# Performance work log

Measured on AMD Instinct MI355X. Metric: run time of the kernel, lower is better.

Reference implementation:

```python
import jax, jax.numpy as jnp
import numpy as np

N, E, H, XD, ED, YD, L = 10000, 640000, 128, 8, 8, 112, 4
EPS_MSG = 1e-7   # GENConv message eps
EPS_SM = 1e-16   # pyg softmax denom eps
EPS_LN = 1e-5    # layernorm eps


def node_ln(x, g, b):
    # torch.nn.LayerNorm over last dim
    m = x.mean(axis=-1, keepdims=True)
    v = x.var(axis=-1, keepdims=True)
    return (x - m) * jax.lax.rsqrt(v + EPS_LN) * g + b


def graph_ln(x, g, b):
    # pyg LayerNorm mode='graph' (no batch): global mean/std over all nodes+channels
    xc = x - x.mean()
    std = jnp.sqrt((xc * xc).mean())
    return xc / (std + EPS_LN) * g + b


def setup_inputs() -> dict:
    key = jax.random.key(0)
    ks = jax.random.split(key, 10)
    rn = lambda k, s, sc: jax.random.normal(k, s, jnp.float32) * sc
    return {
        "x": jax.random.normal(ks[0], (N, XD), jnp.float32),
        "edge_index": jax.random.randint(ks[1], (2, E), 0, N),
        "edge_attr": jax.random.normal(ks[2], (E, ED), jnp.float32),
        "Wn": rn(ks[3], (XD, H), 0.3), "bn": jnp.zeros((H,), jnp.float32),
        "We": rn(ks[4], (ED, H), 0.3), "be": jnp.zeros((H,), jnp.float32),
        "t": jnp.ones((L,), jnp.float32),
        "W1": rn(ks[5], (L, H, 2 * H), 0.08), "b1": jnp.zeros((L, 2 * H), jnp.float32),
        "g1": jnp.ones((L, 2 * H), jnp.float32), "bt1": jnp.zeros((L, 2 * H), jnp.float32),
        "W2": rn(ks[6], (L, 2 * H, H), 0.08), "b2": jnp.zeros((L, H), jnp.float32),
        "lng": jnp.ones((L, H), jnp.float32), "lnb": jnp.zeros((L, H), jnp.float32),
        "Wout": rn(ks[7], (H, YD), 0.08), "bout": jnp.zeros((YD,), jnp.float32),
    }


def reference(x, edge_index, edge_attr, Wn, bn, We, be, t, W1, b1, g1, bt1,
              W2, b2, lng, lnb, Wout, bout):
    src, dst = edge_index[0], edge_index[1]
    h = x @ Wn + bn                       # [N,H] node encoder
    ea = edge_attr @ We + be              # [E,H] edge encoder

    def gen_conv(h, i):
        msg = jax.nn.relu(h[src] + ea) + EPS_MSG          # [E,H]
        logit = msg * t[i]
        mx = jax.ops.segment_max(logit, dst, num_segments=N)
        ex = jnp.exp(logit - mx[dst])
        den = jax.ops.segment_sum(ex, dst, num_segments=N)
        alpha = ex / (den[dst] + EPS_SM)
        agg = jax.ops.segment_sum(alpha * msg, dst, num_segments=N) + h  # root add
        z = jax.nn.relu(graph_ln(agg @ W1[i] + b1[i], g1[i], bt1[i]))
        return z @ W2[i] + b2[i]

    h = gen_conv(h, 0)                    # first layer: conv only
    for i in range(1, L):                 # res+ blocks (dropout off: eval)
        r = jax.nn.relu(node_ln(h, lng[i], lnb[i]))
        h = h + gen_conv(r, i)
    h = jax.nn.relu(node_ln(h, lng[0], lnb[0]))  # layers[0].act(layers[0].norm(x))
    return h @ Wout + bout
```

## Files before the change

kernel.cpp:

```cpp
#include <hip/hip_runtime.h>
#include <math.h>

#define NN 10000
#define NE 640000
#define H 128
#define H2 256
#define XD 8
#define ED 8
#define YD 112
#define NL 4
#define EPS_MSG 1e-7f
#define EPS_SM 1e-16f
#define EPS_LN 1e-5f
#define TN 16
#define NB1 (NN / TN)

__global__ void hist_k(const int* __restrict__ dst, int* __restrict__ counts) {
    int e = blockIdx.x * 256 + threadIdx.x;
    if (e < NE) atomicAdd(&counts[dst[e]], 1);
}

__global__ void scan_k(const int* __restrict__ counts, int* __restrict__ rowptr) {
    __shared__ int part[1024];
    int tid = threadIdx.x;
    const int CH = (NN + 1023) / 1024;
    int base = tid * CH;
    int s = 0;
    for (int j = 0; j < CH; j++) { int i = base + j; if (i < NN) s += counts[i]; }
    part[tid] = s; __syncthreads();
    for (int off = 1; off < 1024; off <<= 1) {
        int v = (tid >= off) ? part[tid - off] : 0;
        __syncthreads();
        part[tid] += v;
        __syncthreads();
    }
    int run = part[tid] - s;
    for (int j = 0; j < CH; j++) {
        int i = base + j;
        if (i < NN) { rowptr[i] = run; run += counts[i]; }
    }
    if (tid == 1023) rowptr[NN] = run;
}

__global__ void scatter_k(const int* __restrict__ src, const int* __restrict__ dst,
                          const float* __restrict__ eattr, const int* __restrict__ rowptr,
                          int* __restrict__ fill, int* __restrict__ srcs,
                          _Float16* __restrict__ eacsr) {
    int e = blockIdx.x * 256 + threadIdx.x;
    if (e >= NE) return;
    int d = dst[e];
    int pos = rowptr[d] + atomicAdd(&fill[d], 1);
    srcs[pos] = src[e];
    const float4* ein = (const float4*)eattr;
    float4 a = ein[(size_t)e * 2];
    float4 b = ein[(size_t)e * 2 + 1];
    float4 pack;
    _Float16* pp = (_Float16*)&pack;
    pp[0] = (_Float16)a.x; pp[1] = (_Float16)a.y; pp[2] = (_Float16)a.z; pp[3] = (_Float16)a.w;
    pp[4] = (_Float16)b.x; pp[5] = (_Float16)b.y; pp[6] = (_Float16)b.z; pp[7] = (_Float16)b.w;
    ((float4*)eacsr)[pos] = pack;
}

__global__ void node_enc_k(const float* __restrict__ x, const float* __restrict__ Wn,
                           const float* __restrict__ bn, float* __restrict__ h) {
    int n = blockIdx.x, c = threadIdx.x;
    __shared__ float xl[XD];
    if (c < XD) xl[c] = x[n * XD + c];
    __syncthreads();
    float acc = bn[c];
#pragma unroll
    for (int k = 0; k < XD; k++) acc = fmaf(xl[k], Wn[k * H + c], acc);
    h[(size_t)n * H + c] = acc;
}

__global__ void __launch_bounds__(128) edge_agg_k(
    const float* __restrict__ rin, const int* __restrict__ rowptr,
    const int* __restrict__ srcs, const _Float16* __restrict__ eacsr,
    const float* __restrict__ We, const float* __restrict__ be,
    const float* __restrict__ tptr, int layer, float* __restrict__ agg) {
    int n = blockIdx.x, c = threadIdx.x;
    float wc[ED];
#pragma unroll
    for (int k = 0; k < ED; k++) wc[k] = We[k * H + c];
    float bec = be[c];
    float ts2 = tptr[layer] * 1.44269504088896f;
    int beg = rowptr[n], end = rowptr[n + 1];
    float rv = rin[(size_t)n * H + c];
    float den = 0.f, num = 0.f;
#pragma unroll 4
    for (int j = beg; j < end; ++j) {
        int sn = srcs[j];
        float4 raw = *(const float4*)(eacsr + (size_t)j * ED);
        const _Float16* ep = (const _Float16*)&raw;
        float hv = rin[(size_t)sn * H + c];
        float p = bec;
        p = fmaf((float)ep[0], wc[0], p); p = fmaf((float)ep[1], wc[1], p);
        p = fmaf((float)ep[2], wc[2], p); p = fmaf((float)ep[3], wc[3], p);
        p = fmaf((float)ep[4], wc[4], p); p = fmaf((float)ep[5], wc[5], p);
        p = fmaf((float)ep[6], wc[6], p); p = fmaf((float)ep[7], wc[7], p);
        float msg = fmaxf(hv + p, 0.f) + EPS_MSG;
        float pe = __builtin_amdgcn_exp2f(msg * ts2);
        den += pe;
        num = fmaf(pe, msg, num);
    }
    agg[(size_t)n * H + c] = num / (den + EPS_SM) + rv;
}

__global__ void __launch_bounds__(256) mm1_k(const float* __restrict__ agg,
    const float* __restrict__ W1i, const float* __restrict__ b1i,
    float* __restrict__ y1, float* __restrict__ part) {
    int nb = blockIdx.x, o = threadIdx.x;
    int n0 = nb * TN;
    __shared__ float a[TN][H];
    for (int t = o; t < TN * H; t += 256) ((float*)a)[t] = agg[(size_t)n0 * H + t];
    __syncthreads();
    float acc[TN];
#pragma unroll
    for (int i = 0; i < TN; i++) acc[i] = 0.f;
    for (int k = 0; k < H; k++) {
        float w = W1i[k * H2 + o];
#pragma unroll
        for (int i = 0; i < TN; i++) acc[i] = fmaf(a[i][k], w, acc[i]);
    }
    float bo = b1i[o];
    float ps = 0.f, ps2 = 0.f;
#pragma unroll
    for (int i = 0; i < TN; i++) {
        float v = acc[i] + bo;
        y1[(size_t)(n0 + i) * H2 + o] = v;
        ps += v; ps2 += v * v;
    }
#pragma unroll
    for (int off = 32; off; off >>= 1) { ps += __shfl_xor(ps, off); ps2 += __shfl_xor(ps2, off); }
    __shared__ float red[8];
    int w = o >> 6;
    if ((o & 63) == 0) { red[w] = ps; red[4 + w] = ps2; }
    __syncthreads();
    if (o == 0) {
        part[nb * 2]     = red[0] + red[1] + red[2] + red[3];
        part[nb * 2 + 1] = red[4] + red[5] + red[6] + red[7];
    }
}

__global__ void __launch_bounds__(128) mm2_k(const float* __restrict__ y1,
    const float* __restrict__ g1i, const float* __restrict__ bt1i,
    const float* __restrict__ W2i, const float* __restrict__ b2i,
    const float* __restrict__ part, float* __restrict__ h,
    const float* __restrict__ lgp, const float* __restrict__ lbp,
    float* __restrict__ r, int first) {
    int nb = blockIdx.x, o = threadIdx.x;
    int n0 = nb * TN;
    float s = 0.f, s2 = 0.f;
    for (int i = o; i < NB1; i += 128) { s += part[2 * i]; s2 += part[2 * i + 1]; }
#pragma unroll
    for (int off = 32; off; off >>= 1) { s += __shfl_xor(s, off); s2 += __shfl_xor(s2, off); }
    __shared__ float sred[4];
    int w = o >> 6;
    if ((o & 63) == 0) { sred[w] = s; sred[2 + w] = s2; }
    __syncthreads();
    const float M = (float)NN * (float)H2;
    float m = (sred[0] + sred[1]) / M;
    float var = fmaxf((sred[2] + sred[3]) / M - m * m, 0.f);
    float istd = 1.f / (sqrtf(var) + EPS_LN);
    __syncthreads();

    __shared__ float z[TN][H2];
    for (int t = o; t < TN * H2; t += 128) {
        int k = t & 255;
        float v = y1[(size_t)n0 * H2 + t];
        v = (v - m) * istd * g1i[k] + bt1i[k];
        ((float*)z)[t] = fmaxf(v, 0.f);
    }
    __syncthreads();
    float acc[TN];
#pragma unroll
    for (int i = 0; i < TN; i++) acc[i] = 0.f;
    for (int k = 0; k < H2; k++) {
        float wv = W2i[k * H + o];
#pragma unroll
        for (int i = 0; i < TN; i++) acc[i] = fmaf(z[i][k], wv, acc[i]);
    }
    float bo = b2i[o];
    float vv[TN];
#pragma unroll
    for (int i = 0; i < TN; i++) {
        size_t idx = (size_t)(n0 + i) * H + o;
        float v = acc[i] + bo;
        if (!first) v += h[idx];
        h[idx] = v;
        vv[i] = v;
    }
    __shared__ float rs[2][TN], rs2[2][TN];
#pragma unroll
    for (int i = 0; i < TN; i++) {
        float ss = vv[i], ss2 = vv[i] * vv[i];
#pragma unroll
        for (int off = 32; off; off >>= 1) { ss += __shfl_xor(ss, off); ss2 += __shfl_xor(ss2, off); }
        if ((o & 63) == 0) { rs[w][i] = ss; rs2[w][i] = ss2; }
    }
    __syncthreads();
    float gc = lgp[o], bc = lbp[o];
#pragma unroll
    for (int i = 0; i < TN; i++) {
        float S = rs[0][i] + rs[1][i], S2 = rs2[0][i] + rs2[1][i];
        float mn = S * (1.f / H);
        float vr = S2 * (1.f / H) - mn * mn;
        float inv = rsqrtf(vr + EPS_LN);
        float ov = (vv[i] - mn) * inv * gc + bc;
        r[(size_t)(n0 + i) * H + o] = fmaxf(ov, 0.f);
    }
}

__global__ void __launch_bounds__(128) mmout_k(const float* __restrict__ r,
    const float* __restrict__ Wout, const float* __restrict__ bout,
    float* __restrict__ out) {
    int nb = blockIdx.x, o = threadIdx.x;
    int n0 = nb * TN;
    __shared__ float a[TN][H];
    for (int t = o; t < TN * H; t += 128) ((float*)a)[t] = r[(size_t)n0 * H + t];
    __syncthreads();
    if (o < YD) {
        float acc[TN];
#pragma unroll
        for (int i = 0; i < TN; i++) acc[i] = 0.f;
        for (int k = 0; k < H; k++) {
            float w = Wout[k * YD + o];
#pragma unroll
            for (int i = 0; i < TN; i++) acc[i] = fmaf(a[i][k], w, acc[i]);
        }
        float bo = bout[o];
#pragma unroll
        for (int i = 0; i < TN; i++) out[(size_t)(n0 + i) * YD + o] = acc[i] + bo;
    }
}

extern "C" void kernel_launch(void* const* d_in, const int* in_sizes, int n_in,
                              void* d_out, int out_size, void* d_ws, size_t ws_size,
                              hipStream_t stream) {
    const float* x    = (const float*)d_in[0];
    const int*   ei   = (const int*)d_in[1];
    const float* eattr= (const float*)d_in[2];
    const float* Wn   = (const float*)d_in[3];
    const float* bn   = (const float*)d_in[4];
    const float* We   = (const float*)d_in[5];
    const float* be   = (const float*)d_in[6];
    const float* t    = (const float*)d_in[7];
    const float* W1   = (const float*)d_in[8];
    const float* b1   = (const float*)d_in[9];
    const float* g1   = (const float*)d_in[10];
    const float* bt1  = (const float*)d_in[11];
    const float* W2   = (const float*)d_in[12];
    const float* b2   = (const float*)d_in[13];
    const float* lng  = (const float*)d_in[14];
    const float* lnb  = (const float*)d_in[15];
    const float* Wout = (const float*)d_in[16];
    const float* bout = (const float*)d_in[17];
    float* out = (float*)d_out;

    const int* src = ei;
    const int* dst = ei + NE;

    char* ws = (char*)d_ws;
    size_t off = 0;
    auto alloc = [&](size_t bytes) -> char* {
        char* p = ws + off;
        off += (bytes + 255) & ~(size_t)255;
        return p;
    };
    int*      counts = (int*)alloc((size_t)NN * 4);
    int*      fill   = (int*)alloc((size_t)NN * 4);
    int*      rowptr = (int*)alloc((size_t)(NN + 1) * 4);
    int*      srcs   = (int*)alloc((size_t)NE * 4);
    _Float16* eacsr  = (_Float16*)alloc((size_t)NE * ED * 2);
    float*    h      = (float*)alloc((size_t)NN * H * 4);
    float*    r      = (float*)alloc((size_t)NN * H * 4);
    float*    agg    = (float*)alloc((size_t)NN * H * 4);
    float*    y1     = (float*)alloc((size_t)NN * H2 * 4);
    float*    part   = (float*)alloc((size_t)NB1 * 2 * 4);
    (void)ws_size; (void)in_sizes; (void)n_in; (void)out_size;

    hipMemsetAsync(counts, 0, (size_t)NN * 4, stream);
    hipMemsetAsync(fill,   0, (size_t)NN * 4, stream);

    hist_k<<<(NE + 255) / 256, 256, 0, stream>>>(dst, counts);
    scan_k<<<1, 1024, 0, stream>>>(counts, rowptr);
    scatter_k<<<(NE + 255) / 256, 256, 0, stream>>>(src, dst, eattr, rowptr, fill,
                                                    srcs, eacsr);
    node_enc_k<<<NN, H, 0, stream>>>(x, Wn, bn, h);

    for (int i = 0; i < NL; i++) {
        const float* cin = (i == 0) ? h : r;
        edge_agg_k<<<NN, H, 0, stream>>>(cin, rowptr, srcs, eacsr, We, be, t, i, agg);
        mm1_k<<<NB1, 256, 0, stream>>>(agg, W1 + (size_t)i * H * H2, b1 + i * H2, y1, part);
        int nx = (i == NL - 1) ? 0 : (i + 1);
        mm2_k<<<NB1, 128, 0, stream>>>(y1, g1 + i * H2, bt1 + i * H2,
                                       W2 + (size_t)i * H2 * H, b2 + i * H, part, h,
                                       lng + nx * H, lnb + nx * H, r, (i == 0) ? 1 : 0);
    }
    mmout_k<<<NB1, 128, 0, stream>>>(r, Wout, bout, out);
}
```

Measured before the change: 580.1 us.

## Halve node tile for dense layers and split mm2 rows across 256 threads

```diff
diff --git a/kernel.cpp b/kernel.cpp
--- a/kernel.cpp
+++ b/kernel.cpp
@@ -12,8 +12,10 @@
 #define EPS_MSG 1e-7f
 #define EPS_SM 1e-16f
 #define EPS_LN 1e-5f
-#define TN 16
-#define NB1 (NN / TN)
+#define TM 8
+#define NB1 (NN / TM)
+#define TNO 16
+#define NBO (NN / TNO)
 
 __global__ void hist_k(const int* __restrict__ dst, int* __restrict__ counts) {
     int e = blockIdx.x * 256 + threadIdx.x;
@@ -110,22 +112,22 @@
     const float* __restrict__ W1i, const float* __restrict__ b1i,
     float* __restrict__ y1, float* __restrict__ part) {
     int nb = blockIdx.x, o = threadIdx.x;
-    int n0 = nb * TN;
-    __shared__ float a[TN][H];
-    for (int t = o; t < TN * H; t += 256) ((float*)a)[t] = agg[(size_t)n0 * H + t];
-    __syncthreads();
-    float acc[TN];
-#pragma unroll
-    for (int i = 0; i < TN; i++) acc[i] = 0.f;
+    int n0 = nb * TM;
+    __shared__ float a[TM][H];
+    for (int t = o; t < TM * H; t += 256) ((float*)a)[t] = agg[(size_t)n0 * H + t];
+    __syncthreads();
+    float acc[TM];
+#pragma unroll
+    for (int i = 0; i < TM; i++) acc[i] = 0.f;
     for (int k = 0; k < H; k++) {
         float w = W1i[k * H2 + o];
 #pragma unroll
-        for (int i = 0; i < TN; i++) acc[i] = fmaf(a[i][k], w, acc[i]);
+        for (int i = 0; i < TM; i++) acc[i] = fmaf(a[i][k], w, acc[i]);
     }
     float bo = b1i[o];
     float ps = 0.f, ps2 = 0.f;
 #pragma unroll
-    for (int i = 0; i < TN; i++) {
+    for (int i = 0; i < TM; i++) {
         float v = acc[i] + bo;
         y1[(size_t)(n0 + i) * H2 + o] = v;
         ps += v; ps2 += v * v;
@@ -142,72 +144,76 @@
     }
 }
 
-__global__ void __launch_bounds__(128) mm2_k(const float* __restrict__ y1,
+__global__ void __launch_bounds__(256) mm2_k(const float* __restrict__ y1,
     const float* __restrict__ g1i, const float* __restrict__ bt1i,
     const float* __restrict__ W2i, const float* __restrict__ b2i,
     const float* __restrict__ part, float* __restrict__ h,
     const float* __restrict__ lgp, const float* __restrict__ lbp,
     float* __restrict__ r, int first) {
-    int nb = blockIdx.x, o = threadIdx.x;
-    int n0 = nb * TN;
+    int nb = blockIdx.x, tid = threadIdx.x;
+    int o = tid & 127, half = tid >> 7;
+    int rb = half * 4;
+    int n0 = nb * TM;
     float s = 0.f, s2 = 0.f;
-    for (int i = o; i < NB1; i += 128) { s += part[2 * i]; s2 += part[2 * i + 1]; }
+    for (int i = tid; i < NB1; i += 256) { s += part[2 * i]; s2 += part[2 * i + 1]; }
 #pragma unroll
     for (int off = 32; off; off >>= 1) { s += __shfl_xor(s, off); s2 += __shfl_xor(s2, off); }
-    __shared__ float sred[4];
-    int w = o >> 6;
-    if ((o & 63) == 0) { sred[w] = s; sred[2 + w] = s2; }
+    __shared__ float sred[8];
+    int w4 = tid >> 6;
+    if ((tid & 63) == 0) { sred[w4] = s; sred[4 + w4] = s2; }
     __syncthreads();
     const float M = (float)NN * (float)H2;
-    float m = (sred[0] + sred[1]) / M;
-    float var = fmaxf((sred[2] + sred[3]) / M - m * m, 0.f);
+    float m = (sred[0] + sred[1] + sred[2] + sred[3]) / M;
+    float var = fmaxf((sred[4] + sred[5] + sred[6] + sred[7]) / M - m * m, 0.f);
     float istd = 1.f / (sqrtf(var) + EPS_LN);
-    __syncthreads();
-
-    __shared__ float z[TN][H2];
-    for (int t = o; t < TN * H2; t += 128) {
+
+    __shared__ float z[TM][H2];
+    __syncthreads();
+    for (int t = tid; t < TM * H2; t += 256) {
         int k = t & 255;
         float v = y1[(size_t)n0 * H2 + t];
         v = (v - m) * istd * g1i[k] + bt1i[k];
         ((float*)z)[t] = fmaxf(v, 0.f);
     }
     __syncthreads();
-    float acc[TN];
-#pragma unroll
-    for (int i = 0; i < TN; i++) acc[i] = 0.f;
+    float acc[4];
+#pragma unroll
+    for (int i = 0; i < 4; i++) acc[i] = 0.f;
     for (int k = 0; k < H2; k++) {
         float wv = W2i[k * H + o];
 #pragma unroll
-        for (int i = 0; i < TN; i++) acc[i] = fmaf(z[i][k], wv, acc[i]);
+        for (int i = 0; i < 4; i++) acc[i] = fmaf(z[rb + i][k], wv, acc[i]);
     }
     float bo = b2i[o];
-    float vv[TN];
-#pragma unroll
-    for (int i = 0; i < TN; i++) {
-        size_t idx = (size_t)(n0 + i) * H + o;
+    float vv[4];
+#pragma unroll
+    for (int i = 0; i < 4; i++) {
+        size_t idx = (size_t)(n0 + rb + i) * H + o;
         float v = acc[i] + bo;
         if (!first) v += h[idx];
         h[idx] = v;
         vv[i] = v;
     }
-    __shared__ float rs[2][TN], rs2[2][TN];
-#pragma unroll
-    for (int i = 0; i < TN; i++) {
+    __shared__ float rs[2][2][4], rs2[2][2][4];
+    int w2 = (tid >> 6) & 1;
+#pragma unroll
+    for (int i = 0; i < 4; i++) {
         float ss = vv[i], ss2 = vv[i] * vv[i];
 #pragma unroll
         for (int off = 32; off; off >>= 1) { ss += __shfl_xor(ss, off); ss2 += __shfl_xor(ss2, off); }
-        if ((o & 63) == 0) { rs[w][i] = ss; rs2[w][i] = ss2; }
+        if ((tid & 63) == 0) { rs[half][w2][i] = ss; rs2[half][w2][i] = ss2; }
     }
     __syncthreads();
     float gc = lgp[o], bc = lbp[o];
 #pragma unroll
-    for (int i = 0; i < TN; i++) {
-        float S = rs[0][i] + rs[1][i], S2 = rs2[0][i] + rs2[1][i];
+    for (int i = 0; i < 4; i++) {
+        float S = rs[half][0][i] + rs[half][1][i];
+        float S2 = rs2[half][0][i] + rs2[half][1][i];
         float mn = S * (1.f / H);
         float vr = S2 * (1.f / H) - mn * mn;
         float inv = rsqrtf(vr + EPS_LN);
         float ov = (vv[i] - mn) * inv * gc + bc;
-        r[(size_t)(n0 + i) * H + o] = fmaxf(ov, 0.f);
+        r[(size_t)(n0 + rb + i) * H + o] = fmaxf(ov, 0.f);
     }
 }
 
@@ -215,22 +221,22 @@
     const float* __restrict__ Wout, const float* __restrict__ bout,
     float* __restrict__ out) {
     int nb = blockIdx.x, o = threadIdx.x;
-    int n0 = nb * TN;
-    __shared__ float a[TN][H];
-    for (int t = o; t < TN * H; t += 128) ((float*)a)[t] = r[(size_t)n0 * H + t];
+    int n0 = nb * TNO;
+    __shared__ float a[TNO][H];
+    for (int t = o; t < TNO * H; t += 128) ((float*)a)[t] = r[(size_t)n0 * H + t];
     __syncthreads();
     if (o < YD) {
-        float acc[TN];
-#pragma unroll
-        for (int i = 0; i < TN; i++) acc[i] = 0.f;
+        float acc[TNO];
+#pragma unroll
+        for (int i = 0; i < TNO; i++) acc[i] = 0.f;
         for (int k = 0; k < H; k++) {
             float w = Wout[k * YD + o];
 #pragma unroll
-            for (int i = 0; i < TN; i++) acc[i] = fmaf(a[i][k], w, acc[i]);
+            for (int i = 0; i < TNO; i++) acc[i] = fmaf(a[i][k], w, acc[i]);
         }
         float bo = bout[o];
 #pragma unroll
-        for (int i = 0; i < TN; i++) out[(size_t)(n0 + i) * YD + o] = acc[i] + bo;
+        for (int i = 0; i < TNO; i++) out[(size_t)(n0 + i) * YD + o] = acc[i] + bo;
     }
 }
 
@@ -293,9 +299,9 @@
         edge_agg_k<<<NN, H, 0, stream>>>(cin, rowptr, srcs, eacsr, We, be, t, i, agg);
         mm1_k<<<NB1, 256, 0, stream>>>(agg, W1 + (size_t)i * H * H2, b1 + i * H2, y1, part);
         int nx = (i == NL - 1) ? 0 : (i + 1);
-        mm2_k<<<NB1, 128, 0, stream>>>(y1, g1 + i * H2, bt1 + i * H2,
+        mm2_k<<<NB1, 256, 0, stream>>>(y1, g1 + i * H2, bt1 + i * H2,
                                        W2 + (size_t)i * H2 * H, b2 + i * H, part, h,
                                        lng + nx * H, lnb + nx * H, r, (i == 0) ? 1 : 0);
     }
-    mmout_k<<<NB1, 128, 0, stream>>>(r, Wout, bout, out);
-}
+    mmout_k<<<NBO, 128, 0, stream>>>(r, Wout, bout, out);
+}
```

New measurement: 490.9 us. -15.4%, faster.
